# Performance work log

Hardware: AMD Instinct MI355X
Metric: run time of the kernel (lower is better)

Reference implementation:

```python
import jax, jax.numpy as jnp
import numpy as np

B, P, T = 128, 196, 20
VOCAB, ENC, EMB, DEC, ATTN = 10000, 2048, 512, 512, 512


def _linear_params(key, out_dim, in_dim):
    kw, kb = jax.random.split(key)
    s = 1.0 / np.sqrt(in_dim)
    W = jax.random.uniform(kw, (out_dim, in_dim), minval=-s, maxval=s, dtype=jnp.float32)
    b = jax.random.uniform(kb, (out_dim,), minval=-s, maxval=s, dtype=jnp.float32)
    return W, b


def setup_inputs() -> dict:
    key = jax.random.key(0)
    ks = jax.random.split(key, 12)
    enc_w, enc_b = _linear_params(ks[0], ATTN, ENC)
    dec_w, dec_b = _linear_params(ks[1], ATTN, DEC)
    full_w, full_b = _linear_params(ks[2], 1, ATTN)
    W_ih, b_ih = _linear_params(ks[3], 4 * DEC, EMB + ENC)
    W_hh, b_hh = _linear_params(ks[4], 4 * DEC, DEC)
    ih_w, ih_b = _linear_params(ks[5], DEC, ENC)
    ic_w, ic_b = _linear_params(ks[6], DEC, ENC)
    fc_w, fc_b = _linear_params(ks[7], VOCAB, DEC)
    return {
        "encoder_out": jax.random.normal(ks[8], (B, P, ENC), dtype=jnp.float32),
        "captions": jax.random.randint(ks[9], (B, T), 0, VOCAB, dtype=jnp.int32),
        "lengths": jax.random.randint(ks[10], (B,), 1, T + 1, dtype=jnp.int32),
        "embedding": jax.random.normal(ks[11], (VOCAB, EMB), dtype=jnp.float32),
        "enc_attn_w": enc_w, "enc_attn_b": enc_b,
        "dec_attn_w": dec_w, "dec_attn_b": dec_b,
        "full_attn_w": full_w, "full_attn_b": full_b,
        "W_ih": W_ih, "b_ih": b_ih, "W_hh": W_hh, "b_hh": b_hh,
        "init_h_w": ih_w, "init_h_b": ih_b,
        "init_c_w": ic_w, "init_c_b": ic_b,
        "fc_w": fc_w, "fc_b": fc_b,
    }


def reference(encoder_out, captions, lengths, embedding,
              enc_attn_w, enc_attn_b, dec_attn_w, dec_attn_b,
              full_attn_w, full_attn_b, W_ih, b_ih, W_hh, b_hh,
              init_h_w, init_h_b, init_c_w, init_c_b, fc_w, fc_b):
    # init hidden state from mean-pooled encoder features
    mean_enc = encoder_out.mean(axis=1)                      # [B, ENC]
    h = mean_enc @ init_h_w.T + init_h_b                      # [B, DEC]
    c = mean_enc @ init_c_w.T + init_c_b

    # loop-invariant encoder projection for additive attention
    attn_enc = jnp.einsum('bpe,ae->bpa', encoder_out, enc_attn_w) + enc_attn_b  # [B, P, ATTN]

    embs = embedding[captions]                                # [B, T, EMB]
    embs_t = jnp.swapaxes(embs, 0, 1)                         # [T, B, EMB]

    dec = h.shape[1]

    def step(carry, emb_t):
        h, c = carry
        # additive attention
        attn_dec = h @ dec_attn_w.T + dec_attn_b              # [B, ATTN]
        energy = jnp.einsum('bpa,a->bp', jax.nn.relu(attn_enc + attn_dec[:, None, :]), full_attn_w[0]) + full_attn_b[0]
        alpha = jax.nn.softmax(energy, axis=1)                # [B, P]
        context = jnp.einsum('bpe,bp->be', encoder_out, alpha)  # [B, ENC]
        # LSTMCell
        x = jnp.concatenate([emb_t, context], axis=1)
        gates = x @ W_ih.T + b_ih + h @ W_hh.T + b_hh          # [B, 4*DEC]
        i, f, g, o = jnp.split(gates, 4, axis=1)
        c_new = jax.nn.sigmoid(f) * c + jax.nn.sigmoid(i) * jnp.tanh(g)
        h_new = jax.nn.sigmoid(o) * jnp.tanh(c_new)
        preds = h_new @ fc_w.T + fc_b                          # [B, VOCAB] (dropout in eval mode = identity)
        return (h_new, c_new), (preds, alpha)

    (_, _), (outputs_t, alphas_t) = jax.lax.scan(step, (h, c), embs_t)
    outputs = jnp.swapaxes(outputs_t, 0, 1)                   # [B, T, VOCAB]
    alphas = jnp.swapaxes(alphas_t, 0, 1)                     # [B, T, P]
    return outputs, alphas
```

## Files before the change

kernel.cpp:

```cpp
#include <hip/hip_runtime.h>

constexpr int kB = 128, kP = 196, kT = 20;
constexpr int kVocab = 10000, kEnc = 2048, kEmb = 512, kDec = 512, kAttn = 512;

typedef __bf16 b16x8 __attribute__((ext_vector_type(8)));
typedef __bf16 b16x4 __attribute__((ext_vector_type(4)));
typedef float f32x4 __attribute__((ext_vector_type(4)));
typedef unsigned short u16x4 __attribute__((ext_vector_type(4)));

__device__ __forceinline__ unsigned short f2bf(float f) {
  unsigned int u = __float_as_uint(f);
  u += 0x7fffu + ((u >> 16) & 1u);
  return (unsigned short)(u >> 16);
}
__device__ __forceinline__ float bf2f(unsigned short h) {
  return __uint_as_float(((unsigned int)h) << 16);
}

__device__ __forceinline__ void async16(const void* g, void* l) {
  __builtin_amdgcn_global_load_lds(
      (const __attribute__((address_space(1))) unsigned int*)g,
      (__attribute__((address_space(3))) unsigned int*)l, 16, 0, 0);
}

template <int MODE>
__global__ __launch_bounds__(256) void gemm128(
    const unsigned short* __restrict__ A, const unsigned short* __restrict__ W,
    const float* __restrict__ bias, unsigned short* __restrict__ Cb,
    float* __restrict__ Cf, int K, int Nv) {
  __shared__ unsigned short sA[2][128 * 32];
  __shared__ unsigned short sB[2][128 * 32];
  const int tid = threadIdx.x;
  const int lane = tid & 63, wave = tid >> 6;
  const int wm = wave >> 1, wn = wave & 1;
  const int q = lane >> 4, l = lane & 15;
  const int nwg = gridDim.x * gridDim.y;
  const int orig = blockIdx.y * gridDim.x + blockIdx.x;
  const int qc = nwg >> 3, rc = nwg & 7;
  const int xcd = orig & 7, o8 = orig >> 3;
  const int wg = (xcd < rc ? xcd * (qc + 1) : rc * (qc + 1) + (xcd - rc) * qc) + o8;
  const int m0 = (wg / gridDim.x) * 128, n0 = (wg % gridDim.x) * 128;
  const int row0 = tid & 127, ch0 = tid >> 7;
  const long arow = (long)(m0 + row0) * K + ch0 * 8;
  const long brow = (long)(n0 + row0) * K + ch0 * 8;
  f32x4 acc[4][4] = {};

  auto stage = [&](int buf, int k0) {
    async16(A + arow + k0, &sA[buf][(ch0 * 128 + row0) * 8]);
    async16(A + arow + k0 + 16, &sA[buf][((ch0 + 2) * 128 + row0) * 8]);
    async16(W + brow + k0, &sB[buf][(ch0 * 128 + row0) * 8]);
    async16(W + brow + k0 + 16, &sB[buf][((ch0 + 2) * 128 + row0) * 8]);
  };

  stage(0, 0);
  __syncthreads();
  int cur = 0;
  for (int k0 = 0; k0 < K; k0 += 32) {
    const bool last = (k0 + 32 >= K);
    if (!last) stage(cur ^ 1, k0 + 32);
    b16x8 af[4], bfr[4];
#pragma unroll
    for (int i = 0; i < 4; i++)
      af[i] = *(const b16x8*)&sA[cur][(q * 128 + wm * 64 + 16 * i + l) * 8];
#pragma unroll
    for (int j = 0; j < 4; j++)
      bfr[j] = *(const b16x8*)&sB[cur][(q * 128 + wn * 64 + 16 * j + l) * 8];
#pragma unroll
    for (int i = 0; i < 4; i++)
#pragma unroll
      for (int j = 0; j < 4; j++)
        acc[i][j] = __builtin_amdgcn_mfma_f32_16x16x32_bf16(af[i], bfr[j], acc[i][j], 0, 0, 0);
    if (!last) {
      __syncthreads();
      cur ^= 1;
    }
  }

#pragma unroll
  for (int i = 0; i < 4; i++) {
    const int row = m0 + wm * 64 + 16 * i + q * 4;
#pragma unroll
    for (int j = 0; j < 4; j++) {
      const int col = n0 + wn * 64 + 16 * j + l;
      if (col >= Nv) continue;
      const float bv = bias[col];
#pragma unroll
      for (int r = 0; r < 4; r++) {
        const float v = acc[i][j][r] + bv;
        if (MODE == 0) {
          Cb[(long)(row + r) * kAttn + col] = f2bf(v);
        } else {
          const int rr = row + r;
          Cf[((long)(rr & 127) * kT + (rr >> 7)) * (long)kVocab + col] = v;
        }
      }
    }
  }
}

template <bool A_BF16, bool OUT_BF16>
__global__ __launch_bounds__(256) void gemm_bt(
    const void* __restrict__ A_, const unsigned short* __restrict__ W,
    const float* __restrict__ bias, float* __restrict__ C,
    unsigned short* __restrict__ Cb, int M, int N, int K, long ldc) {
  const int lane = threadIdx.x & 63;
  const int wave = threadIdx.x >> 6;
  const int wm = wave >> 1, wn = wave & 1;
  const int m0 = blockIdx.y * 64 + wm * 32;
  const int n0 = blockIdx.x * 64 + wn * 32;
  const int q = lane >> 4;
  const int l = lane & 15;
  f32x4 acc[2][2] = {};
  const unsigned short* Ab = (const unsigned short*)A_;
  const float* Af = (const float*)A_;

  for (int k0 = 0; k0 < K; k0 += 32) {
    const int ka = k0 + q * 8;
    b16x8 af[2], wf[2];
#pragma unroll
    for (int i = 0; i < 2; i++) {
      int r = m0 + 16 * i + l;
      if (r >= M) r = M - 1;
      if (A_BF16) {
        af[i] = *(const b16x8*)(Ab + (long)r * K + ka);
      } else {
        const float* p = Af + (long)r * K + ka;
        const f32x4 lo = *(const f32x4*)p;
        const f32x4 hi = *(const f32x4*)(p + 4);
        b16x8 t;
#pragma unroll
        for (int j = 0; j < 4; j++) {
          ((unsigned short*)&t)[j] = f2bf(lo[j]);
          ((unsigned short*)&t)[4 + j] = f2bf(hi[j]);
        }
        af[i] = t;
      }
    }
#pragma unroll
    for (int j = 0; j < 2; j++) {
      int r = n0 + 16 * j + l;
      if (r >= N) r = N - 1;
      wf[j] = *(const b16x8*)(W + (long)r * K + ka);
    }
#pragma unroll
    for (int i = 0; i < 2; i++)
#pragma unroll
      for (int j = 0; j < 2; j++)
        acc[i][j] = __builtin_amdgcn_mfma_f32_16x16x32_bf16(af[i], wf[j], acc[i][j], 0, 0, 0);
  }

#pragma unroll
  for (int i = 0; i < 2; i++)
#pragma unroll
    for (int j = 0; j < 2; j++) {
      const int col = n0 + 16 * j + l;
      if (col >= N) continue;
      const float bv = bias ? bias[col] : 0.0f;
#pragma unroll
      for (int r = 0; r < 4; r++) {
        const int row = m0 + 16 * i + q * 4 + r;
        if (row >= M) continue;
        const float v = acc[i][j][r] + bv;
        if (OUT_BF16) Cb[(long)row * ldc + col] = f2bf(v);
        else          C[(long)row * ldc + col] = v;
      }
    }
}

__global__ __launch_bounds__(256) void adfc_kernel(
    const unsigned short* __restrict__ h_bf,
    const unsigned short* __restrict__ daw, const float* __restrict__ dab,
    float* __restrict__ ad_out) {
  const int blk = blockIdx.x;
  const int n0 = (blk & 7) * 64, m0 = (blk >> 3) * 64;
  const int lane = threadIdx.x & 63, wave = threadIdx.x >> 6;
  const int wm = wave >> 1, wn = wave & 1;
  const int q = lane >> 4, l = lane & 15;
  const int mi = m0 + wm * 32, ni = n0 + wn * 32;
  f32x4 acc[2][2] = {};

  for (int k0 = 0; k0 < 512; k0 += 64) {
    b16x8 af[2][2], wf[2][2];
#pragma unroll
    for (int u = 0; u < 2; u++) {
      const int ka = k0 + u * 32 + q * 8;
#pragma unroll
      for (int i = 0; i < 2; i++)
        af[u][i] = *(const b16x8*)(h_bf + (long)(mi + 16 * i + l) * 512 + ka);
#pragma unroll
      for (int j = 0; j < 2; j++)
        wf[u][j] = *(const b16x8*)(daw + (long)(ni + 16 * j + l) * 512 + ka);
    }
#pragma unroll
    for (int u = 0; u < 2; u++)
#pragma unroll
      for (int i = 0; i < 2; i++)
#pragma unroll
        for (int j = 0; j < 2; j++)
          acc[i][j] = __builtin_amdgcn_mfma_f32_16x16x32_bf16(af[u][i], wf[u][j], acc[i][j], 0, 0, 0);
  }
#pragma unroll
  for (int i = 0; i < 2; i++)
#pragma unroll
    for (int j = 0; j < 2; j++) {
      const int col = ni + 16 * j + l;
      const float bv = dab[col];
#pragma unroll
      for (int r = 0; r < 4; r++) {
        const int row = mi + 16 * i + q * 4 + r;
        ad_out[(long)row * 512 + col] = acc[i][j][r] + bv;
      }
    }
}

template <bool SRC_BF16>
__global__ __launch_bounds__(256) void attn2(
    const void* __restrict__ enc_, const unsigned short* __restrict__ attn_enc_bf,
    const float* __restrict__ ad_g, const float* __restrict__ faw,
    const float* __restrict__ fab, float* __restrict__ alphas,
    unsigned short* __restrict__ ctx, int t) {
  const int b = blockIdx.x;
  const int half = blockIdx.y;
  const int tid = threadIdx.x;
  const int lane = tid & 63, wave = tid >> 6;
  __shared__ float ad_s[512];
  __shared__ float e_sm[kP];
  __shared__ float red[4];
  __shared__ float cred[128][8];

  ad_s[tid] = ad_g[b * kAttn + tid];
  ad_s[tid + 256] = ad_g[b * kAttn + tid + 256];
  __syncthreads();

  float ad8[8], w8[8];
  const int a0 = lane * 8;
#pragma unroll
  for (int j = 0; j < 8; j++) { ad8[j] = ad_s[a0 + j]; w8[j] = faw[a0 + j]; }
  const float fb0 = fab[0];
  for (int p = wave; p < kP; p += 4) {
    const b16x8 rv = *(const b16x8*)(attn_enc_bf + ((long)(b * kP + p)) * kAttn + a0);
    float s = 0.f;
#pragma unroll
    for (int j = 0; j < 8; j++)
      s += w8[j] * fmaxf(bf2f(((const unsigned short*)&rv)[j]) + ad8[j], 0.f);
#pragma unroll
    for (int off = 32; off > 0; off >>= 1) s += __shfl_down(s, off, 64);
    if (lane == 0) e_sm[p] = s + fb0;
  }
  __syncthreads();

  const float v = (tid < kP) ? e_sm[tid] : -3.0e38f;
  float m = v;
#pragma unroll
  for (int off = 32; off > 0; off >>= 1) m = fmaxf(m, __shfl_down(m, off, 64));
  if (lane == 0) red[wave] = m;
  __syncthreads();
  m = fmaxf(fmaxf(red[0], red[1]), fmaxf(red[2], red[3]));
  const float ex = (tid < kP) ? expf(v - m) : 0.f;
  float s = ex;
#pragma unroll
  for (int off = 32; off > 0; off >>= 1) s += __shfl_down(s, off, 64);
  if (lane == 0) red[wave] = s;
  __syncthreads();
  s = red[0] + red[1] + red[2] + red[3];
  __syncthreads();
  const float alpha = ex / s;
  if (tid < kP) {
    e_sm[tid] = alpha;
    if (half == 0) alphas[((long)b * kT + t) * kP + tid] = alpha;
  }
  __syncthreads();

  const int pg = tid >> 7, th = tid & 127;
  const int e = half * 1024 + th * 8;
  float a8[8] = {};
  if (SRC_BF16) {
    const unsigned short* base = (const unsigned short*)enc_ + (long)b * kP * kEnc + e;
    const int pbeg = pg * 98;
#pragma unroll 2
    for (int p = pbeg; p < pbeg + 98; p++) {
      const float a = e_sm[p];
      const b16x8 rv = *(const b16x8*)(base + (long)p * kEnc);
#pragma unroll
      for (int j = 0; j < 8; j++) a8[j] += a * bf2f(((const unsigned short*)&rv)[j]);
    }
  } else {
    const float* base = (const float*)enc_ + (long)b * kP * kEnc + e;
    const int pbeg = pg * 98;
#pragma unroll 2
    for (int p = pbeg; p < pbeg + 98; p++) {
      const float a = e_sm[p];
      const f32x4 lo = *(const f32x4*)(base + (long)p * kEnc);
      const f32x4 hi = *(const f32x4*)(base + (long)p * kEnc + 4);
#pragma unroll
      for (int j = 0; j < 4; j++) { a8[j] += a * lo[j]; a8[4 + j] += a * hi[j]; }
    }
  }
  if (pg == 1) {
#pragma unroll
    for (int j = 0; j < 8; j++) cred[th][j] = a8[j];
  }
  __syncthreads();
  if (pg == 0) {
    u16x4 o0, o1;
#pragma unroll
    for (int j = 0; j < 4; j++) {
      o0[j] = f2bf(a8[j] + cred[th][j]);
      o1[j] = f2bf(a8[4 + j] + cred[th][4 + j]);
    }
    *(u16x4*)(ctx + (long)b * kEnc + e) = o0;
    *(u16x4*)(ctx + (long)b * kEnc + e + 4) = o1;
  }
}

__global__ __launch_bounds__(256) void gemm_gates(
    const unsigned short* __restrict__ embs_t, const unsigned short* __restrict__ ctx,
    const unsigned short* __restrict__ hbf, const unsigned short* __restrict__ Wih,
    const unsigned short* __restrict__ Whh, float* __restrict__ gates_part) {
  const int lane = threadIdx.x & 63;
  const int wave = threadIdx.x >> 6;
  const int wm = wave >> 1, wn = wave & 1;
  const int m0 = blockIdx.y * 64 + wm * 32;
  const int n0 = blockIdx.x * 64 + wn * 32;
  const int z = blockIdx.z;
  const int q = lane >> 4;
  const int l = lane & 15;
  f32x4 acc[2][2] = {};
  float* gout = gates_part + (long)z * kB * 2048;

  const int kbeg = z * 768, kend = kbeg + 768;
  for (int k0 = kbeg; k0 < kend; k0 += 32) {
    b16x8 af[2], wf[2];
#pragma unroll
    for (int i = 0; i < 2; i++) {
      const int r = m0 + 16 * i + l;
      const unsigned short* p;
      if (k0 < 512)        p = embs_t + (long)r * kEmb + k0;
      else if (k0 < 2560)  p = ctx + (long)r * kEnc + (k0 - 512);
      else                 p = hbf + (long)r * kDec + (k0 - 2560);
      af[i] = *(const b16x8*)(p + q * 8);
    }
#pragma unroll
    for (int j = 0; j < 2; j++) {
      const int r = n0 + 16 * j + l;
      const unsigned short* p;
      if (k0 < 2560) p = Wih + (long)r * 2560 + k0;
      else           p = Whh + (long)r * 512 + (k0 - 2560);
      wf[j] = *(const b16x8*)(p + q * 8);
    }
#pragma unroll
    for (int i = 0; i < 2; i++)
#pragma unroll
      for (int j = 0; j < 2; j++)
        acc[i][j] = __builtin_amdgcn_mfma_f32_16x16x32_bf16(af[i], wf[j], acc[i][j], 0, 0, 0);
  }
#pragma unroll
  for (int i = 0; i < 2; i++)
#pragma unroll
    for (int j = 0; j < 2; j++) {
      const int col = n0 + 16 * j + l;
#pragma unroll
      for (int r = 0; r < 4; r++) {
        const int row = m0 + 16 * i + q * 4 + r;
        gout[(long)row * 2048 + col] = acc[i][j][r];
      }
    }
}

__global__ __launch_bounds__(256) void lstm_ad(
    const float* __restrict__ gp, const float* __restrict__ bsum,
    float* __restrict__ c, unsigned short* __restrict__ h_out,
    const unsigned short* __restrict__ daw, const float* __restrict__ dab,
    float* __restrict__ ad_out) {
  const int b = blockIdx.x;
  const int tid = threadIdx.x;
  __shared__ unsigned short h_s[512];

#pragma unroll
  for (int u = 0; u < 2; u++) {
    const int d = tid + u * 256;
    float g4[4];
#pragma unroll
    for (int g = 0; g < 4; g++) {
      const int col = g * 512 + d;
      float s = bsum[col];
#pragma unroll
      for (int z = 0; z < 4; z++) s += gp[(long)z * kB * 2048 + (long)b * 2048 + col];
      g4[g] = s;
    }
    const float si = 1.f / (1.f + expf(-g4[0]));
    const float sf = 1.f / (1.f + expf(-g4[1]));
    const float so = 1.f / (1.f + expf(-g4[3]));
    const long idx = (long)b * 512 + d;
    const float cn = sf * c[idx] + si * tanhf(g4[2]);
    const float hn = so * tanhf(cn);
    c[idx] = cn;
    const unsigned short hb = f2bf(hn);
    h_out[idx] = hb;
    h_s[d] = hb;
  }
  __syncthreads();

#pragma unroll
  for (int u = 0; u < 2; u++) {
    const int r = tid + u * 256;
    const unsigned short* wr = daw + (long)r * 512;
    float s = 0.f;
    for (int k = 0; k < 512; k += 8) {
      const b16x8 hv = *(const b16x8*)&h_s[k];
      const b16x8 wv = *(const b16x8*)(wr + k);
#pragma unroll
      for (int j = 0; j < 8; j++)
        s += bf2f(((const unsigned short*)&hv)[j]) * bf2f(((const unsigned short*)&wv)[j]);
    }
    ad_out[(long)b * 512 + r] = s + dab[r];
  }
}

template <bool SRC_BF16>
__global__ __launch_bounds__(256) void mean_kernel(
    const void* __restrict__ enc_, unsigned short* __restrict__ mean_bf) {
  const int b = blockIdx.x;
  const int e = threadIdx.x * 8;
  float acc[8] = {};
  if (SRC_BF16) {
    const unsigned short* base = (const unsigned short*)enc_ + (long)b * kP * kEnc + e;
    for (int p = 0; p < kP; p++) {
      const b16x8 v = *(const b16x8*)(base + (long)p * kEnc);
#pragma unroll
      for (int j = 0; j < 8; j++) acc[j] += bf2f(((const unsigned short*)&v)[j]);
    }
  } else {
    const float* base = (const float*)enc_ + (long)b * kP * kEnc + e;
    for (int p = 0; p < kP; p++) {
      const f32x4 lo = *(const f32x4*)(base + (long)p * kEnc);
      const f32x4 hi = *(const f32x4*)(base + (long)p * kEnc + 4);
#pragma unroll
      for (int j = 0; j < 4; j++) { acc[j] += lo[j]; acc[4 + j] += hi[j]; }
    }
  }
#pragma unroll
  for (int j = 0; j < 8; j++)
    mean_bf[(long)b * kEnc + e + j] = f2bf(acc[j] * (1.0f / 196.0f));
}

__global__ __launch_bounds__(256) void f32_to_bf16_vec(
    const float* __restrict__ src, unsigned short* __restrict__ dst, long n4) {
  for (long i = blockIdx.x * (long)blockDim.x + threadIdx.x; i < n4;
       i += (long)gridDim.x * blockDim.x) {
    const f32x4 v = *(const f32x4*)(src + i * 4);
    u16x4 o;
#pragma unroll
    for (int j = 0; j < 4; j++) o[j] = f2bf(v[j]);
    *(u16x4*)(dst + i * 4) = o;
  }
}

__global__ __launch_bounds__(256) void gather_emb(
    const float* __restrict__ embedding, const int* __restrict__ captions,
    unsigned short* __restrict__ embs) {
  const int r = blockIdx.x;
  const int t = r >> 7, b = r & 127;
  const int cap = captions[b * kT + t];
  const float* src = embedding + (long)cap * kEmb;
  unsigned short* dst = embs + (long)r * kEmb;
  for (int i = threadIdx.x; i < kEmb; i += 256) dst[i] = f2bf(src[i]);
}

__global__ void bias_sum_k(const float* __restrict__ b1, const float* __restrict__ b2,
                           float* __restrict__ o) {
  const int i = blockIdx.x * 256 + threadIdx.x;
  if (i < 2048) o[i] = b1[i] + b2[i];
}

extern "C" void kernel_launch(void* const* d_in, const int* in_sizes, int n_in,
                              void* d_out, int out_size, void* d_ws, size_t ws_size,
                              hipStream_t stream) {
  const float* enc = (const float*)d_in[0];
  const int* captions = (const int*)d_in[1];
  const float* embedding = (const float*)d_in[3];
  const float* eaw = (const float*)d_in[4];
  const float* eab = (const float*)d_in[5];
  const float* daw = (const float*)d_in[6];
  const float* dab = (const float*)d_in[7];
  const float* faw = (const float*)d_in[8];
  const float* fab = (const float*)d_in[9];
  const float* Wih = (const float*)d_in[10];
  const float* bih = (const float*)d_in[11];
  const float* Whh = (const float*)d_in[12];
  const float* bhh = (const float*)d_in[13];
  const float* ihw = (const float*)d_in[14];
  const float* ihb = (const float*)d_in[15];
  const float* icw = (const float*)d_in[16];
  const float* icb = (const float*)d_in[17];
  const float* fcw = (const float*)d_in[18];
  const float* fcb = (const float*)d_in[19];

  float* out = (float*)d_out;
  float* alphas = out + (long)kB * kT * kVocab;

  char* ws = (char*)d_ws;
  size_t off = 0;
  auto alloc = [&](size_t bytes) -> void* {
    void* p = ws + off;
    off = (off + bytes + 255) & ~(size_t)255;
    return p;
  };
  unsigned short* attn_enc_bf = (unsigned short*)alloc((size_t)kB * kP * kAttn * 2);
  unsigned short* Wih_bf = (unsigned short*)alloc((size_t)2048 * 2560 * 2);
  unsigned short* Whh_bf = (unsigned short*)alloc((size_t)2048 * 512 * 2);
  unsigned short* fcw_bf = (unsigned short*)alloc((size_t)kVocab * kDec * 2);
  unsigned short* eaw_bf = (unsigned short*)alloc((size_t)kAttn * kEnc * 2);
  unsigned short* daw_bf = (unsigned short*)alloc((size_t)kAttn * kDec * 2);
  unsigned short* ihw_bf = (unsigned short*)alloc((size_t)kDec * kEnc * 2);
  unsigned short* icw_bf = (unsigned short*)alloc((size_t)kDec * kEnc * 2);
  unsigned short* embs_bf = (unsigned short*)alloc((size_t)kT * kB * kEmb * 2);
  unsigned short* mean_bf = (unsigned short*)alloc((size_t)kB * kEnc * 2);
  float* h = (float*)alloc((size_t)kB * kDec * 4);
  float* c = (float*)alloc((size_t)kB * kDec * 4);
  unsigned short* h_hist = (unsigned short*)alloc((size_t)(kT + 1) * kB * kDec * 2);
  float* ad_buf = (float*)alloc((size_t)kB * kAttn * 4);
  unsigned short* ctx_bf = (unsigned short*)alloc((size_t)kB * kEnc * 2);
  float* gates_part = (float*)alloc((size_t)4 * kB * 2048 * 4);
  float* bsum = (float*)alloc((size_t)2048 * 4);
  unsigned short* enc_bf = (unsigned short*)alloc((size_t)kB * kP * kEnc * 2);
  const bool have_enc_bf = (off <= ws_size);

  auto cvt = [&](const float* s, unsigned short* d, long n) {
    const long n4 = n / 4;
    long g = (n4 + 255) / 256;
    if (g > 2048) g = 2048;
    f32_to_bf16_vec<<<dim3((unsigned)g), dim3(256), 0, stream>>>(s, d, n4);
  };

  cvt(eaw, eaw_bf, (long)kAttn * kEnc);
  cvt(daw, daw_bf, (long)kAttn * kDec);
  cvt(Wih, Wih_bf, (long)2048 * 2560);
  cvt(Whh, Whh_bf, (long)2048 * 512);
  cvt(fcw, fcw_bf, (long)kVocab * kDec);
  cvt(ihw, ihw_bf, (long)kDec * kEnc);
  cvt(icw, icw_bf, (long)kDec * kEnc);
  if (have_enc_bf) cvt(enc, enc_bf, (long)kB * kP * kEnc);
  bias_sum_k<<<8, 256, 0, stream>>>(bih, bhh, bsum);
  gather_emb<<<kT * kB, 256, 0, stream>>>(embedding, captions, embs_bf);
  if (have_enc_bf)
    mean_kernel<true><<<kB, 256, 0, stream>>>(enc_bf, mean_bf);
  else
    mean_kernel<false><<<kB, 256, 0, stream>>>(enc, mean_bf);

  gemm_bt<true, false><<<dim3(kDec / 64, kB / 64), 256, 0, stream>>>(
      mean_bf, ihw_bf, ihb, h, (unsigned short*)nullptr, kB, kDec, kEnc, kDec);
  gemm_bt<true, false><<<dim3(kDec / 64, kB / 64), 256, 0, stream>>>(
      mean_bf, icw_bf, icb, c, (unsigned short*)nullptr, kB, kDec, kEnc, kDec);
  cvt(h, h_hist, (long)kB * kDec);

  if (have_enc_bf)
    gemm128<0><<<dim3(kAttn / 128, (kB * kP) / 128), 256, 0, stream>>>(
        enc_bf, eaw_bf, eab, attn_enc_bf, (float*)nullptr, kEnc, kAttn);
  else
    gemm_bt<false, true><<<dim3(kAttn / 64, (kB * kP) / 64), 256, 0, stream>>>(
        enc, eaw_bf, eab, (float*)nullptr, attn_enc_bf, kB * kP, kAttn, kEnc, kAttn);

  adfc_kernel<<<16, 256, 0, stream>>>(h_hist, daw_bf, dab, ad_buf);

  for (int t = 0; t < kT; t++) {
    const unsigned short* hcur = h_hist + (long)t * kB * kDec;

    if (have_enc_bf)
      attn2<true><<<dim3(kB, 2), 256, 0, stream>>>(
          enc_bf, attn_enc_bf, ad_buf, faw, fab, alphas, ctx_bf, t);
    else
      attn2<false><<<dim3(kB, 2), 256, 0, stream>>>(
          enc, attn_enc_bf, ad_buf, faw, fab, alphas, ctx_bf, t);

    gemm_gates<<<dim3(2048 / 64, kB / 64, 4), 256, 0, stream>>>(
        embs_bf + (long)t * kB * kEmb, ctx_bf, hcur, Wih_bf, Whh_bf, gates_part);

    lstm_ad<<<kB, 256, 0, stream>>>(
        gates_part, bsum, c, h_hist + (long)(t + 1) * kB * kDec, daw_bf, dab, ad_buf);
  }

  gemm128<1><<<dim3((kVocab + 127) / 128, kT * kB / 128), 256, 0, stream>>>(
      h_hist + (long)kB * kDec, fcw_bf, fcb, (unsigned short*)nullptr, out, kDec, kVocab);
}
```

Before: 2.366 ms.

## Fuse encoder conversion with mean pooling and batch loads across attention and GEMMs

A new mean_cvt kernel converts encoder_out to bf16 and computes the mean in one pass, replacing a separate conversion and a mean kernel that reread the bf16 copy. The gemm128 K-tile grows from 32 to 64, the attention energy and context loops batch several row loads before computing, and gemm_gates unrolls K by two. The init-h GEMM writes bf16 directly into h_hist, dropping a float buffer and a conversion launch. The decoder projection keeps h in float shared memory and uses four partial accumulators. These changes aim to raise memory-level parallelism and remove redundant passes, at the cost of more registers and shared memory (64 KB in gemm128).

```diff
diff --git a/kernel.cpp b/kernel.cpp
--- a/kernel.cpp
+++ b/kernel.cpp
@@ -28,8 +28,8 @@
     const unsigned short* __restrict__ A, const unsigned short* __restrict__ W,
     const float* __restrict__ bias, unsigned short* __restrict__ Cb,
     float* __restrict__ Cf, int K, int Nv) {
-  __shared__ unsigned short sA[2][128 * 32];
-  __shared__ unsigned short sB[2][128 * 32];
+  __shared__ unsigned short sA[2][128 * 64];
+  __shared__ unsigned short sB[2][128 * 64];
   const int tid = threadIdx.x;
   const int lane = tid & 63, wave = tid >> 6;
   const int wm = wave >> 1, wn = wave & 1;
@@ -41,35 +41,43 @@
   const int wg = (xcd < rc ? xcd * (qc + 1) : rc * (qc + 1) + (xcd - rc) * qc) + o8;
   const int m0 = (wg / gridDim.x) * 128, n0 = (wg % gridDim.x) * 128;
   const int row0 = tid & 127, ch0 = tid >> 7;
-  const long arow = (long)(m0 + row0) * K + ch0 * 8;
-  const long brow = (long)(n0 + row0) * K + ch0 * 8;
+  const long arow = (long)(m0 + row0) * K;
+  const long brow = (long)(n0 + row0) * K;
   f32x4 acc[4][4] = {};
 
   auto stage = [&](int buf, int k0) {
-    async16(A + arow + k0, &sA[buf][(ch0 * 128 + row0) * 8]);
-    async16(A + arow + k0 + 16, &sA[buf][((ch0 + 2) * 128 + row0) * 8]);
-    async16(W + brow + k0, &sB[buf][(ch0 * 128 + row0) * 8]);
-    async16(W + brow + k0 + 16, &sB[buf][((ch0 + 2) * 128 + row0) * 8]);
+#pragma unroll
+    for (int cc = 0; cc < 4; cc++) {
+      const int ch = ch0 + cc * 2;
+      async16(A + arow + k0 + ch * 8, &sA[buf][(ch * 128 + row0) * 8]);
+      async16(W + brow + k0 + ch * 8, &sB[buf][(ch * 128 + row0) * 8]);
+    }
   };
 
   stage(0, 0);
   __syncthreads();
   int cur = 0;
-  for (int k0 = 0; k0 < K; k0 += 32) {
-    const bool last = (k0 + 32 >= K);
-    if (!last) stage(cur ^ 1, k0 + 32);
-    b16x8 af[4], bfr[4];
-#pragma unroll
-    for (int i = 0; i < 4; i++)
-      af[i] = *(const b16x8*)&sA[cur][(q * 128 + wm * 64 + 16 * i + l) * 8];
-#pragma unroll
-    for (int j = 0; j < 4; j++)
-      bfr[j] = *(const b16x8*)&sB[cur][(q * 128 + wn * 64 + 16 * j + l) * 8];
-#pragma unroll
-    for (int i = 0; i < 4; i++)
+  for (int k0 = 0; k0 < K; k0 += 64) {
+    const bool last = (k0 + 64 >= K);
+    if (!last) stage(cur ^ 1, k0 + 64);
+    b16x8 af[2][4], bfr[2][4];
+#pragma unroll
+    for (int u = 0; u < 2; u++) {
+      const int cb = u * 4 + q;
+#pragma unroll
+      for (int i = 0; i < 4; i++)
+        af[u][i] = *(const b16x8*)&sA[cur][(cb * 128 + wm * 64 + 16 * i + l) * 8];
 #pragma unroll
       for (int j = 0; j < 4; j++)
-        acc[i][j] = __builtin_amdgcn_mfma_f32_16x16x32_bf16(af[i], bfr[j], acc[i][j], 0, 0, 0);
+        bfr[u][j] = *(const b16x8*)&sB[cur][(cb * 128 + wn * 64 + 16 * j + l) * 8];
+    }
+#pragma unroll
+    for (int u = 0; u < 2; u++)
+#pragma unroll
+      for (int i = 0; i < 4; i++)
+#pragma unroll
+        for (int j = 0; j < 4; j++)
+          acc[i][j] = __builtin_amdgcn_mfma_f32_16x16x32_bf16(af[u][i], bfr[u][j], acc[i][j], 0, 0, 0);
     if (!last) {
       __syncthreads();
       cur ^= 1;
@@ -237,15 +245,41 @@
 #pragma unroll
   for (int j = 0; j < 8; j++) { ad8[j] = ad_s[a0 + j]; w8[j] = faw[a0 + j]; }
   const float fb0 = fab[0];
-  for (int p = wave; p < kP; p += 4) {
-    const b16x8 rv = *(const b16x8*)(attn_enc_bf + ((long)(b * kP + p)) * kAttn + a0);
-    float s = 0.f;
-#pragma unroll
-    for (int j = 0; j < 8; j++)
-      s += w8[j] * fmaxf(bf2f(((const unsigned short*)&rv)[j]) + ad8[j], 0.f);
-#pragma unroll
-    for (int off = 32; off > 0; off >>= 1) s += __shfl_down(s, off, 64);
-    if (lane == 0) e_sm[p] = s + fb0;
+  {
+    int p = wave;
+#pragma unroll 1
+    for (int it = 0; it < 12; it++, p += 16) {
+      b16x8 rv[4];
+#pragma unroll
+      for (int u = 0; u < 4; u++)
+        rv[u] = *(const b16x8*)(attn_enc_bf + ((long)(b * kP + p + 4 * u)) * kAttn + a0);
+      float s4[4];
+#pragma unroll
+      for (int u = 0; u < 4; u++) {
+        float s = 0.f;
+#pragma unroll
+        for (int j = 0; j < 8; j++)
+          s += w8[j] * fmaxf(bf2f(((const unsigned short*)&rv[u])[j]) + ad8[j], 0.f);
+        s4[u] = s;
+      }
+#pragma unroll
+      for (int u = 0; u < 4; u++) {
+        float s = s4[u];
+#pragma unroll
+        for (int off = 32; off > 0; off >>= 1) s += __shfl_down(s, off, 64);
+        if (lane == 0) e_sm[p + 4 * u] = s + fb0;
+      }
+    }
+    {
+      const b16x8 rv = *(const b16x8*)(attn_enc_bf + ((long)(b * kP + p)) * kAttn + a0);
+      float s = 0.f;
+#pragma unroll
+      for (int j = 0; j < 8; j++)
+        s += w8[j] * fmaxf(bf2f(((const unsigned short*)&rv)[j]) + ad8[j], 0.f);
+#pragma unroll
+      for (int off = 32; off > 0; off >>= 1) s += __shfl_down(s, off, 64);
+      if (lane == 0) e_sm[p] = s + fb0;
+    }
   }
   __syncthreads();
 
@@ -276,9 +310,21 @@
   float a8[8] = {};
   if (SRC_BF16) {
     const unsigned short* base = (const unsigned short*)enc_ + (long)b * kP * kEnc + e;
-    const int pbeg = pg * 98;
-#pragma unroll 2
-    for (int p = pbeg; p < pbeg + 98; p++) {
+    int p = pg * 98;
+#pragma unroll 1
+    for (int it = 0; it < 12; it++, p += 8) {
+      b16x8 rv[8];
+#pragma unroll
+      for (int u = 0; u < 8; u++) rv[u] = *(const b16x8*)(base + (long)(p + u) * kEnc);
+#pragma unroll
+      for (int u = 0; u < 8; u++) {
+        const float a = e_sm[p + u];
+#pragma unroll
+        for (int j = 0; j < 8; j++) a8[j] += a * bf2f(((const unsigned short*)&rv[u])[j]);
+      }
+    }
+#pragma unroll
+    for (int u = 0; u < 2; u++, p++) {
       const float a = e_sm[p];
       const b16x8 rv = *(const b16x8*)(base + (long)p * kEnc);
 #pragma unroll
@@ -329,30 +375,36 @@
   float* gout = gates_part + (long)z * kB * 2048;
 
   const int kbeg = z * 768, kend = kbeg + 768;
-  for (int k0 = kbeg; k0 < kend; k0 += 32) {
-    b16x8 af[2], wf[2];
-#pragma unroll
-    for (int i = 0; i < 2; i++) {
-      const int r = m0 + 16 * i + l;
-      const unsigned short* p;
-      if (k0 < 512)        p = embs_t + (long)r * kEmb + k0;
-      else if (k0 < 2560)  p = ctx + (long)r * kEnc + (k0 - 512);
-      else                 p = hbf + (long)r * kDec + (k0 - 2560);
-      af[i] = *(const b16x8*)(p + q * 8);
-    }
-#pragma unroll
-    for (int j = 0; j < 2; j++) {
-      const int r = n0 + 16 * j + l;
-      const unsigned short* p;
-      if (k0 < 2560) p = Wih + (long)r * 2560 + k0;
-      else           p = Whh + (long)r * 512 + (k0 - 2560);
-      wf[j] = *(const b16x8*)(p + q * 8);
-    }
-#pragma unroll
-    for (int i = 0; i < 2; i++)
-#pragma unroll
-      for (int j = 0; j < 2; j++)
-        acc[i][j] = __builtin_amdgcn_mfma_f32_16x16x32_bf16(af[i], wf[j], acc[i][j], 0, 0, 0);
+  for (int k0 = kbeg; k0 < kend; k0 += 64) {
+    b16x8 af[2][2], wf[2][2];
+#pragma unroll
+    for (int u = 0; u < 2; u++) {
+      const int k = k0 + u * 32;
+#pragma unroll
+      for (int i = 0; i < 2; i++) {
+        const int r = m0 + 16 * i + l;
+        const unsigned short* p;
+        if (k < 512)        p = embs_t + (long)r * kEmb + k;
+        else if (k < 2560)  p = ctx + (long)r * kEnc + (k - 512);
+        else                p = hbf + (long)r * kDec + (k - 2560);
+        af[u][i] = *(const b16x8*)(p + q * 8);
+      }
+#pragma unroll
+      for (int j = 0; j < 2; j++) {
+        const int r = n0 + 16 * j + l;
+        const unsigned short* p;
+        if (k < 2560) p = Wih + (long)r * 2560 + k;
+        else          p = Whh + (long)r * 512 + (k - 2560);
+        wf[u][j] = *(const b16x8*)(p + q * 8);
+      }
+    }
+#pragma unroll
+    for (int u = 0; u < 2; u++)
+#pragma unroll
+      for (int i = 0; i < 2; i++)
+#pragma unroll
+        for (int j = 0; j < 2; j++)
+          acc[i][j] = __builtin_amdgcn_mfma_f32_16x16x32_bf16(af[u][i], wf[u][j], acc[i][j], 0, 0, 0);
   }
 #pragma unroll
   for (int i = 0; i < 2; i++)
@@ -374,7 +426,7 @@
     float* __restrict__ ad_out) {
   const int b = blockIdx.x;
   const int tid = threadIdx.x;
-  __shared__ unsigned short h_s[512];
+  __shared__ float h_s[512];
 
 #pragma unroll
   for (int u = 0; u < 2; u++) {
@@ -397,7 +449,7 @@
     c[idx] = cn;
     const unsigned short hb = f2bf(hn);
     h_out[idx] = hb;
-    h_s[d] = hb;
+    h_s[d] = bf2f(hb);
   }
   __syncthreads();
 
@@ -405,16 +457,51 @@
   for (int u = 0; u < 2; u++) {
     const int r = tid + u * 256;
     const unsigned short* wr = daw + (long)r * 512;
-    float s = 0.f;
-    for (int k = 0; k < 512; k += 8) {
-      const b16x8 hv = *(const b16x8*)&h_s[k];
-      const b16x8 wv = *(const b16x8*)(wr + k);
-#pragma unroll
-      for (int j = 0; j < 8; j++)
-        s += bf2f(((const unsigned short*)&hv)[j]) * bf2f(((const unsigned short*)&wv)[j]);
-    }
-    ad_out[(long)b * 512 + r] = s + dab[r];
-  }
+    float s0 = 0.f, s1 = 0.f, s2 = 0.f, s3 = 0.f;
+#pragma unroll 1
+    for (int k = 0; k < 512; k += 32) {
+      b16x8 wv[4];
+#pragma unroll
+      for (int v = 0; v < 4; v++) wv[v] = *(const b16x8*)(wr + k + v * 8);
+#pragma unroll
+      for (int j = 0; j < 8; j++) s0 += h_s[k + j]      * bf2f(((const unsigned short*)&wv[0])[j]);
+#pragma unroll
+      for (int j = 0; j < 8; j++) s1 += h_s[k + 8 + j]  * bf2f(((const unsigned short*)&wv[1])[j]);
+#pragma unroll
+      for (int j = 0; j < 8; j++) s2 += h_s[k + 16 + j] * bf2f(((const unsigned short*)&wv[2])[j]);
+#pragma unroll
+      for (int j = 0; j < 8; j++) s3 += h_s[k + 24 + j] * bf2f(((const unsigned short*)&wv[3])[j]);
+    }
+    ad_out[(long)b * 512 + r] = ((s0 + s1) + (s2 + s3)) + dab[r];
+  }
+}
+
+__global__ __launch_bounds__(256) void mean_cvt(
+    const float* __restrict__ enc, unsigned short* __restrict__ enc_bf,
+    unsigned short* __restrict__ mean_bf) {
+  const int b = blockIdx.x;
+  const int e = blockIdx.y * 1024 + threadIdx.x * 4;
+  const float* base = enc + (long)b * kP * kEnc + e;
+  unsigned short* ob = enc_bf + (long)b * kP * kEnc + e;
+  f32x4 acc = {};
+  int p = 0;
+#pragma unroll 1
+  for (int it = 0; it < 49; it++, p += 4) {
+    f32x4 v[4];
+#pragma unroll
+    for (int u = 0; u < 4; u++) v[u] = *(const f32x4*)(base + (long)(p + u) * kEnc);
+#pragma unroll
+    for (int u = 0; u < 4; u++) {
+      u16x4 o;
+#pragma unroll
+      for (int j = 0; j < 4; j++) { acc[j] += v[u][j]; o[j] = f2bf(v[u][j]); }
+      *(u16x4*)(ob + (long)(p + u) * kEnc) = o;
+    }
+  }
+  u16x4 om;
+#pragma unroll
+  for (int j = 0; j < 4; j++) om[j] = f2bf(acc[j] * (1.0f / 196.0f));
+  *(u16x4*)(mean_bf + (long)b * kEnc + e) = om;
 }
 
 template <bool SRC_BF16>
@@ -516,7 +603,6 @@
   unsigned short* icw_bf = (unsigned short*)alloc((size_t)kDec * kEnc * 2);
   unsigned short* embs_bf = (unsigned short*)alloc((size_t)kT * kB * kEmb * 2);
   unsigned short* mean_bf = (unsigned short*)alloc((size_t)kB * kEnc * 2);
-  float* h = (float*)alloc((size_t)kB * kDec * 4);
   float* c = (float*)alloc((size_t)kB * kDec * 4);
   unsigned short* h_hist = (unsigned short*)alloc((size_t)(kT + 1) * kB * kDec * 2);
   float* ad_buf = (float*)alloc((size_t)kB * kAttn * 4);
@@ -540,19 +626,17 @@
   cvt(fcw, fcw_bf, (long)kVocab * kDec);
   cvt(ihw, ihw_bf, (long)kDec * kEnc);
   cvt(icw, icw_bf, (long)kDec * kEnc);
-  if (have_enc_bf) cvt(enc, enc_bf, (long)kB * kP * kEnc);
   bias_sum_k<<<8, 256, 0, stream>>>(bih, bhh, bsum);
   gather_emb<<<kT * kB, 256, 0, stream>>>(embedding, captions, embs_bf);
   if (have_enc_bf)
-    mean_kernel<true><<<kB, 256, 0, stream>>>(enc_bf, mean_bf);
+    mean_cvt<<<dim3(kB, 2), 256, 0, stream>>>(enc, enc_bf, mean_bf);
   else
     mean_kernel<false><<<kB, 256, 0, stream>>>(enc, mean_bf);
 
-  gemm_bt<true, false><<<dim3(kDec / 64, kB / 64), 256, 0, stream>>>(
-      mean_bf, ihw_bf, ihb, h, (unsigned short*)nullptr, kB, kDec, kEnc, kDec);
+  gemm_bt<true, true><<<dim3(kDec / 64, kB / 64), 256, 0, stream>>>(
+      mean_bf, ihw_bf, ihb, (float*)nullptr, h_hist, kB, kDec, kEnc, kDec);
   gemm_bt<true, false><<<dim3(kDec / 64, kB / 64), 256, 0, stream>>>(
       mean_bf, icw_bf, icb, c, (unsigned short*)nullptr, kB, kDec, kEnc, kDec);
-  cvt(h, h_hist, (long)kB * kDec);
 
   if (have_enc_bf)
     gemm128<0><<<dim3(kAttn / 128, (kB * kP) / 128), 256, 0, stream>>>(
```

Measured after the change: 2.125 ms. 1.11x faster.
